# Kernel tuning notes

Measured on AMD Instinct MI355X. Metric: run time of the kernel, lower is better.

## Reference

```python
import jax, jax.numpy as jnp
import numpy as np

B, N, C, H = 8, 4096, 512, 8
DH = C // H
EPS = 1e-12  # torch F.normalize eps


def setup_inputs() -> dict:
    key = jax.random.key(0)
    ks = jax.random.split(key, 5)
    x = jax.random.normal(ks[0], (B, N, C), dtype=jnp.float32)
    y = jax.random.normal(ks[1], (B, N, 256), dtype=jnp.float32)
    kv_w = jax.random.normal(ks[2], (2 * C, C), dtype=jnp.float32) / np.sqrt(C)
    q_w = jax.random.normal(ks[3], (C, 256), dtype=jnp.float32) / np.sqrt(256)
    proj_w = jax.random.normal(ks[4], (C, C), dtype=jnp.float32) / np.sqrt(C)
    proj_b = jnp.zeros((C,), dtype=jnp.float32)
    temperature = jnp.ones((H, 1, 1), dtype=jnp.float32)
    return {"x": x, "y": y, "kv_w": kv_w, "q_w": q_w,
            "proj_w": proj_w, "proj_b": proj_b, "temperature": temperature}


def _l2norm(t):
    # torch F.normalize(dim=-1): t / max(||t||, eps)
    n = jnp.sqrt(jnp.sum(t * t, axis=-1, keepdims=True))
    return t / jnp.maximum(n, EPS)


def reference(x, y, kv_w, q_w, proj_w, proj_b, temperature):
    b, n, c = x.shape
    dh = c // H
    kv = (x @ kv_w.T).reshape(b, n, 2, H, dh)
    k = kv[:, :, 0].transpose(0, 2, 3, 1)  # [B,H,dh,N]
    v = kv[:, :, 1].transpose(0, 2, 3, 1)  # [B,H,dh,N]
    q = (y @ q_w.T).reshape(b, n, H, dh).transpose(0, 2, 3, 1)  # [B,H,dh,N]
    q = _l2norm(q)
    k = _l2norm(k)
    attn = jnp.einsum('bhdn,bhen->bhde', q, k) * temperature  # [B,H,dh,dh]
    attn = jax.nn.softmax(attn, axis=-1)
    out = jnp.einsum('bhde,bhen->bhdn', attn, v)  # [B,H,dh,N]
    out = out.transpose(0, 3, 1, 2).reshape(b, n, c)  # [B,N,C]
    return out @ proj_w.T + proj_b
```

## Files before the change

### kernel.cpp

```cpp
#include <hip/hip_runtime.h>
#include <stdint.h>

typedef unsigned short u16;
typedef unsigned int u32;
typedef __attribute__((ext_vector_type(8))) short bf16x8;
typedef __attribute__((ext_vector_type(4))) float f32x4;

typedef __attribute__((address_space(1))) const u32* gas_p;
typedef __attribute__((address_space(3))) u32* las_p;

__device__ __forceinline__ float bf2f(u16 u) {
    union { u32 u; float f; } v; v.u = ((u32)u) << 16; return v.f;
}
__device__ __forceinline__ u16 f2bf(float f) {
    union { __bf16 b; u16 u; } v; v.b = (__bf16)f; return v.u;
}
__device__ __forceinline__ uint4 cvt8(float4 a, float4 b) {
    union { u16 h[8]; uint4 v; } o;
    o.h[0] = f2bf(a.x); o.h[1] = f2bf(a.y); o.h[2] = f2bf(a.z); o.h[3] = f2bf(a.w);
    o.h[4] = f2bf(b.x); o.h[5] = f2bf(b.y); o.h[6] = f2bf(b.z); o.h[7] = f2bf(b.w);
    return o.v;
}
__device__ __forceinline__ void gl_lds16(const u16* g, u16* l) {
    __builtin_amdgcn_global_load_lds((gas_p)g, (las_p)l, 16, 0, 0);
}
__device__ __forceinline__ bool is_f32(const void* tp) {
    return *(const u32*)tp == 0x3F800000u;
}

__launch_bounds__(256)
__global__ void convert_inputs(const void* __restrict__ kvwi, const void* __restrict__ qwi,
                               const void* __restrict__ pwi, const void* __restrict__ pbi,
                               const void* __restrict__ tpi,
                               u16* __restrict__ kvwb, u16* __restrict__ qwb,
                               u16* __restrict__ pwb, u16* __restrict__ pbb,
                               float* __restrict__ tempf)
{
    const bool f32m = is_f32(tpi);
    long c = (long)blockIdx.x * 256 + threadIdx.x;
    const void* src; u16* dst; long local;
    if      (c < 65536)  { src = kvwi; dst = kvwb; local = c; }
    else if (c < 81920)  { src = qwi;  dst = qwb;  local = c - 65536; }
    else if (c < 114688) { src = pwi;  dst = pwb;  local = c - 81920; }
    else if (c < 114752) { src = pbi;  dst = pbb;  local = c - 114688; }
    else if (c == 114752) {
        for (int i = 0; i < 8; i++)
            tempf[i] = f32m ? ((const float*)tpi)[i] : bf2f(((const u16*)tpi)[i]);
        return;
    } else return;

    long e0 = local * 8;
    if (f32m) {
        const float* s = (const float*)src + e0;
        *(uint4*)(dst + e0) = cvt8(*(const float4*)s, *(const float4*)(s + 4));
    } else {
        *(uint4*)(dst + e0) = *(const uint4*)((const u16*)src + e0);
    }
}

__launch_bounds__(256)
__global__ void gemm_qkT(const void* __restrict__ xv, const void* __restrict__ yv,
                         const u16* __restrict__ kvwb, const u16* __restrict__ qwb,
                         u16* __restrict__ qT, u16* __restrict__ kT,
                         const void* __restrict__ tp)
{
    __shared__ __align__(16) u16 smem[17408];
    u16 (*As)[128][32] = (u16(*)[128][32])smem;
    u16 (*Bs)[128][32] = (u16(*)[128][32])(smem + 8192);

    const int id = blockIdx.x;
    const int xcd = id & 7, j = id >> 3;
    const int z = j >> 7, jj = j & 127;
    const int n0 = (jj & 3) * 128;
    const int m0 = (xcd * 32 + (jj >> 2)) * 128;

    const void* Av = z ? xv : yv;
    const u16* Bw  = z ? kvwb : qwb;
    u16* T         = z ? kT : qT;
    const int K    = z ? 512 : 256;

    const bool f32m = is_f32(tp);
    const int t  = threadIdx.x;
    const int w = t >> 6, lane = t & 63, quad = lane >> 4, l16 = lane & 15;
    const int wm = (w >> 1) * 64, wn = (w & 1) * 64;

    f32x4 acc[4][4];
#pragma unroll
    for (int i = 0; i < 4; i++)
#pragma unroll
        for (int jx = 0; jx < 4; jx++) acc[i][jx] = (f32x4){0.f, 0.f, 0.f, 0.f};

    const int slot = t & 3, srow = t >> 2;
    const int csw = (slot ^ ((t >> 3) & 3)) * 8;
    const int dst = slot * 8;
    const int qsw = (quad ^ ((l16 >> 1) & 3)) * 8;

    const float* Af = (const float*)Av;
    const u16*   Ab = (const u16*)Av;
    const long a0r = (long)(m0 + srow) * K + csw;
    const long a1r = (long)(m0 + srow + 64) * K + csw;
    const long b0r = (long)(n0 + srow) * K + csw;
    const long b1r = (long)(n0 + srow + 64) * K + csw;

    if (f32m) {
        float4 p0 = *(const float4*)&Af[a0r], p1 = *(const float4*)&Af[a0r + 4];
        float4 p2 = *(const float4*)&Af[a1r], p3 = *(const float4*)&Af[a1r + 4];
        *(uint4*)&As[0][srow][dst]      = cvt8(p0, p1);
        *(uint4*)&As[0][srow + 64][dst] = cvt8(p2, p3);
    } else {
        gl_lds16(&Ab[a0r], &As[0][srow][dst]);
        gl_lds16(&Ab[a1r], &As[0][srow + 64][dst]);
    }
    gl_lds16(&Bw[b0r], &Bs[0][srow][dst]);
    gl_lds16(&Bw[b1r], &Bs[0][srow + 64][dst]);
    __syncthreads();

    const int nk = K >> 5;
    for (int kk = 0; kk < nk; kk++) {
        const int cur = kk & 1, nxt = cur ^ 1;
        const int k1 = (kk + 1) << 5;
        const bool more = (kk + 1 < nk);
        float4 la0, la1, lb0, lb1;
        if (more) {
            if (f32m) {
                la0 = *(const float4*)&Af[a0r + k1];
                la1 = *(const float4*)&Af[a0r + k1 + 4];
                lb0 = *(const float4*)&Af[a1r + k1];
                lb1 = *(const float4*)&Af[a1r + k1 + 4];
            } else {
                gl_lds16(&Ab[a0r + k1], &As[nxt][srow][dst]);
                gl_lds16(&Ab[a1r + k1], &As[nxt][srow + 64][dst]);
            }
            gl_lds16(&Bw[b0r + k1], &Bs[nxt][srow][dst]);
            gl_lds16(&Bw[b1r + k1], &Bs[nxt][srow + 64][dst]);
        }
        bf16x8 af[4], bfv[4];
#pragma unroll
        for (int i = 0; i < 4; i++) af[i]  = *(const bf16x8*)&As[cur][wm + i * 16 + l16][qsw];
#pragma unroll
        for (int jx = 0; jx < 4; jx++) bfv[jx] = *(const bf16x8*)&Bs[cur][wn + jx * 16 + l16][qsw];
#pragma unroll
        for (int i = 0; i < 4; i++)
#pragma unroll
            for (int jx = 0; jx < 4; jx++)
                acc[i][jx] = __builtin_amdgcn_mfma_f32_16x16x32_bf16(af[i], bfv[jx], acc[i][jx], 0, 0, 0);
        if (more && f32m) {
            *(uint4*)&As[nxt][srow][dst]      = cvt8(la0, la1);
            *(uint4*)&As[nxt][srow + 64][dst] = cvt8(lb0, lb1);
        }
        __syncthreads();
    }

    u16 (*Cs)[136] = (u16(*)[136])smem;
#pragma unroll
    for (int i = 0; i < 4; i++)
#pragma unroll
        for (int jx = 0; jx < 4; jx++)
#pragma unroll
            for (int r = 0; r < 4; r++)
                Cs[wn + jx * 16 + l16][wm + i * 16 + quad * 4 + r] = f2bf(acc[i][jx][r]);
    __syncthreads();
    const int nrow = t >> 1, mh = (t & 1) * 64;
    const int gn = n0 + nrow;
    const int gm = m0 + mh;
    const int bb = gm >> 12, tok = gm & 4095;
    const long tbase = ((long)(bb * 512 + gn)) * 4096 + tok;
#pragma unroll
    for (int v8 = 0; v8 < 8; v8++)
        *(uint4*)&T[tbase + v8 * 8] = *(uint4*)&Cs[nrow][mh + v8 * 8];
}

__launch_bounds__(256)
__global__ void gram_kernel(const u16* __restrict__ qT, const u16* __restrict__ kT,
                            float* __restrict__ pQK, float* __restrict__ pDQ,
                            float* __restrict__ pDK)
{
    const int nc = blockIdx.x, bh = blockIdx.y;
    const int t = threadIdx.x, w = t >> 6, lane = t & 63;
    const int quad = lane >> 4, l16 = lane & 15;

    __shared__ float red[4][64][64];
    __shared__ float dql[4][64];
    __shared__ float dkl[4][64];

    const u16* qb = qT + (long)bh * 64 * 4096;
    const u16* kb = kT + (long)bh * 64 * 4096;

    f32x4 g[4][4], gq[4], gk[4];
#pragma unroll
    for (int i = 0; i < 4; i++) {
        gq[i] = (f32x4){0.f, 0.f, 0.f, 0.f};
        gk[i] = (f32x4){0.f, 0.f, 0.f, 0.f};
#pragma unroll
        for (int j = 0; j < 4; j++) g[i][j] = (f32x4){0.f, 0.f, 0.f, 0.f};
    }

#pragma unroll
    for (int ks = 0; ks < 4; ks++) {
        const int n = nc * 512 + w * 128 + ks * 32 + quad * 8;
        bf16x8 aq[4], bk[4];
#pragma unroll
        for (int i = 0; i < 4; i++) aq[i] = *(const bf16x8*)&qb[(long)(i * 16 + l16) * 4096 + n];
#pragma unroll
        for (int j = 0; j < 4; j++) bk[j] = *(const bf16x8*)&kb[(long)(j * 16 + l16) * 4096 + n];
#pragma unroll
        for (int i = 0; i < 4; i++)
#pragma unroll
            for (int j = 0; j < 4; j++)
                g[i][j] = __builtin_amdgcn_mfma_f32_16x16x32_bf16(aq[i], bk[j], g[i][j], 0, 0, 0);
#pragma unroll
        for (int i = 0; i < 4; i++) {
            gq[i] = __builtin_amdgcn_mfma_f32_16x16x32_bf16(aq[i], aq[i], gq[i], 0, 0, 0);
            gk[i] = __builtin_amdgcn_mfma_f32_16x16x32_bf16(bk[i], bk[i], gk[i], 0, 0, 0);
        }
    }

#pragma unroll
    for (int i = 0; i < 4; i++)
#pragma unroll
        for (int j = 0; j < 4; j++)
#pragma unroll
            for (int r = 0; r < 4; r++)
                red[w][i * 16 + quad * 4 + r][j * 16 + l16] = g[i][j][r];
    if ((l16 >> 2) == quad) {
        const int rr = l16 & 3;
#pragma unroll
        for (int i = 0; i < 4; i++) {
            float dq = 0.f, dk = 0.f;
#pragma unroll
            for (int r = 0; r < 4; r++)
                if (r == rr) { dq = gq[i][r]; dk = gk[i][r]; }
            dql[w][i * 16 + l16] = dq;
            dkl[w][i * 16 + l16] = dk;
        }
    }
    __syncthreads();

    const long obase = (long)(nc * 64 + bh);
    const int e = t & 63, d0 = (t >> 6) * 16;
    float* o = pQK + obase * 4096;
#pragma unroll
    for (int dd = 0; dd < 16; dd++) {
        int d = d0 + dd;
        o[d * 64 + e] = red[0][d][e] + red[1][d][e] + red[2][d][e] + red[3][d][e];
    }
    if (t < 64) {
        pDQ[obase * 64 + t] = dql[0][t] + dql[1][t] + dql[2][t] + dql[3][t];
        pDK[obase * 64 + t] = dkl[0][t] + dkl[1][t] + dkl[2][t] + dkl[3][t];
    }
}

__launch_bounds__(256)
__global__ void attn_kernel(const float* __restrict__ pQK, const float* __restrict__ pDQ,
                            const float* __restrict__ pDK, const float* __restrict__ tempf,
                            u16* __restrict__ attnT)
{
    const int bh = blockIdx.x;
    const int t = threadIdx.x, w = t >> 6, l = t & 63;
    __shared__ float G[64][65];
    __shared__ float rq[64], rk[64];

#pragma unroll
    for (int ii = 0; ii < 16; ii++) {
        int i = w * 16 + ii;
        float s = 0.f;
#pragma unroll
        for (int nc = 0; nc < 8; nc++) s += pQK[((long)(nc * 64 + bh)) * 4096 + i * 64 + l];
        G[i][l] = s;
    }
    if (t < 64) {
        float sq = 0.f, sk = 0.f;
#pragma unroll
        for (int nc = 0; nc < 8; nc++) {
            sq += pDQ[(nc * 64 + bh) * 64 + t];
            sk += pDK[(nc * 64 + bh) * 64 + t];
        }
        rq[t] = 1.f / fmaxf(sqrtf(sq), 1e-12f);
        rk[t] = 1.f / fmaxf(sqrtf(sk), 1e-12f);
    }
    __syncthreads();

    if (t < 64) {
        const float invq = tempf[bh & 7] * rq[t];
        float mx = -1e30f;
        float row[64];
#pragma unroll
        for (int e = 0; e < 64; e++) {
            float s = G[t][e] * invq * rk[e];
            row[e] = s;
            mx = fmaxf(mx, s);
        }
        float sum = 0.f;
#pragma unroll
        for (int e = 0; e < 64; e++) {
            float p = __expf(row[e] - mx);
            row[e] = p;
            sum += p;
        }
        float inv = 1.f / sum;
#pragma unroll
        for (int e = 0; e < 64; e++)
            attnT[((long)bh * 64 + e) * 64 + t] = f2bf(row[e] * inv);
    }
}

__launch_bounds__(256)
__global__ void wcomb_kernel(const u16* __restrict__ attnT, const u16* __restrict__ pwb,
                             u16* __restrict__ Wc)
{
    const int cc = blockIdx.x, bh = blockIdx.y;
    const int b = bh >> 3, h = bh & 7;
    const int t = threadIdx.x, w = t >> 6, lane = t & 63;
    const int quad = lane >> 4, l16 = lane & 15;
    const int cb = cc * 128 + w * 32;

    f32x4 acc[2][4];
#pragma unroll
    for (int i = 0; i < 2; i++)
#pragma unroll
        for (int j = 0; j < 4; j++) acc[i][j] = (f32x4){0.f, 0.f, 0.f, 0.f};

#pragma unroll
    for (int ks = 0; ks < 2; ks++) {
        const int k = ks * 32 + quad * 8;
        bf16x8 af[2], bfr[4];
#pragma unroll
        for (int i = 0; i < 2; i++)
            af[i] = *(const bf16x8*)&pwb[(long)(cb + i * 16 + l16) * 512 + h * 64 + k];
#pragma unroll
        for (int j = 0; j < 4; j++)
            bfr[j] = *(const bf16x8*)&attnT[((long)bh * 64 + j * 16 + l16) * 64 + k];
#pragma unroll
        for (int i = 0; i < 2; i++)
#pragma unroll
            for (int j = 0; j < 4; j++)
                acc[i][j] = __builtin_amdgcn_mfma_f32_16x16x32_bf16(af[i], bfr[j], acc[i][j], 0, 0, 0);
    }

#pragma unroll
    for (int i = 0; i < 2; i++)
#pragma unroll
        for (int j = 0; j < 4; j++)
#pragma unroll
            for (int r = 0; r < 4; r++) {
                int c = cb + i * 16 + quad * 4 + r;
                int e = j * 16 + l16;
                Wc[((long)(b * 512 + c)) * 512 + h * 64 + e] = f2bf(acc[i][j][r]);
            }
}

__launch_bounds__(256)
__global__ void transpose_kv(const u16* __restrict__ in, u16* __restrict__ out)
{
    __shared__ __align__(16) u16 ts[64][72];
    const int bx = blockIdx.x * 64;
    const int by = blockIdx.y * 64;
    const int t = threadIdx.x;
    const int r = t >> 3, c0 = (t & 7) * 8;
#pragma unroll
    for (int p = 0; p < 2; p++)
        *(uint4*)&ts[r + p * 32][c0] = *(const uint4*)&in[(long)(by + r + p * 32) * 512 + bx + c0];
    __syncthreads();
#pragma unroll
    for (int p = 0; p < 2; p++) {
        int rr = r + p * 32;
        union { u16 h[8]; uint4 v; } tmp;
#pragma unroll
        for (int c = 0; c < 8; c++) tmp.h[c] = ts[c0 + c][rr];
        *(uint4*)&out[(long)(bx + rr) * 512 + by + c0] = tmp.v;
    }
}

__launch_bounds__(256)
__global__ void gemm_bt(const u16* __restrict__ A, const u16* __restrict__ B,
                        u16* __restrict__ C,
                        int K, long sA, long sB, long sC)
{
    __shared__ __align__(16) u16 smem[17408];
    u16 (*As)[128][32] = (u16(*)[128][32])smem;
    u16 (*Bs)[128][32] = (u16(*)[128][32])(smem + 8192);

    const int id = blockIdx.x;
    const int z = id & 7, jj = id >> 3;
    const int n0 = (jj & 3) * 128;
    const int m0 = (jj >> 2) * 128;
    const int t  = threadIdx.x;
    A += (long)z * sA;
    B += (long)z * sB;
    C += (long)z * sC;

    const int w = t >> 6, lane = t & 63, quad = lane >> 4, l16 = lane & 15;
    const int wm = (w >> 1) * 64, wn = (w & 1) * 64;

    f32x4 acc[4][4];
#pragma unroll
    for (int i = 0; i < 4; i++)
#pragma unroll
        for (int j = 0; j < 4; j++) acc[i][j] = (f32x4){0.f, 0.f, 0.f, 0.f};

    const int slot = t & 3, srow = t >> 2;
    const int csw = (slot ^ ((t >> 3) & 3)) * 8;
    const int dst = slot * 8;
    const int qsw = (quad ^ ((l16 >> 1) & 3)) * 8;

    const long a0r = (long)(m0 + srow) * K + csw;
    const long a1r = (long)(m0 + srow + 64) * K + csw;
    const long b0r = (long)(n0 + srow) * K + csw;
    const long b1r = (long)(n0 + srow + 64) * K + csw;

    gl_lds16(&A[a0r], &As[0][srow][dst]);
    gl_lds16(&A[a1r], &As[0][srow + 64][dst]);
    gl_lds16(&B[b0r], &Bs[0][srow][dst]);
    gl_lds16(&B[b1r], &Bs[0][srow + 64][dst]);
    __syncthreads();

    const int nk = K >> 5;
    for (int kk = 0; kk < nk; kk++) {
        const int cur = kk & 1, nxt = cur ^ 1;
        const int k1 = (kk + 1) << 5;
        if (kk + 1 < nk) {
            gl_lds16(&A[a0r + k1], &As[nxt][srow][dst]);
            gl_lds16(&A[a1r + k1], &As[nxt][srow + 64][dst]);
            gl_lds16(&B[b0r + k1], &Bs[nxt][srow][dst]);
            gl_lds16(&B[b1r + k1], &Bs[nxt][srow + 64][dst]);
        }
        bf16x8 af[4], bfr[4];
#pragma unroll
        for (int i = 0; i < 4; i++) af[i]  = *(const bf16x8*)&As[cur][wm + i * 16 + l16][qsw];
#pragma unroll
        for (int j = 0; j < 4; j++) bfr[j] = *(const bf16x8*)&Bs[cur][wn + j * 16 + l16][qsw];
#pragma unroll
        for (int i = 0; i < 4; i++)
#pragma unroll
            for (int j = 0; j < 4; j++)
                acc[i][j] = __builtin_amdgcn_mfma_f32_16x16x32_bf16(af[i], bfr[j], acc[i][j], 0, 0, 0);
        __syncthreads();
    }

    u16 (*Cs)[136] = (u16(*)[136])smem;
#pragma unroll
    for (int i = 0; i < 4; i++)
#pragma unroll
        for (int j = 0; j < 4; j++) {
            int nn = wn + j * 16 + l16;
#pragma unroll
            for (int r = 0; r < 4; r++)
                Cs[wm + i * 16 + quad * 4 + r][nn] = f2bf(acc[i][j][r]);
        }
    __syncthreads();
    const int row = t >> 1, c0 = (t & 1) * 64;
#pragma unroll
    for (int v8 = 0; v8 < 8; v8++)
        *(uint4*)&C[(long)(m0 + row) * 512 + n0 + c0 + v8 * 8] = *(uint4*)&Cs[row][c0 + v8 * 8];
}

__launch_bounds__(256)
__global__ void gemm_out(const void* __restrict__ Av, const u16* __restrict__ B,
                         void* __restrict__ Cv, const u16* __restrict__ bias,
                         const void* __restrict__ tp)
{
    __shared__ __align__(16) u16 smem[17408];
    u16 (*As)[128][32] = (u16(*)[128][32])smem;
    u16 (*Bs)[128][32] = (u16(*)[128][32])(smem + 8192);

    const bool f32m = is_f32(tp);
    const int id = blockIdx.x;
    const int z = id & 7, jj = id >> 3;
    const int n0 = (jj & 3) * 128;
    const int m0 = (jj >> 2) * 128;
    const int t  = threadIdx.x;
    const long aoff = (long)z * 4096 * 512;
    B += (long)z * 512 * 512;

    const int w = t >> 6, lane = t & 63, quad = lane >> 4, l16 = lane & 15;
    const int wm = (w >> 1) * 64, wn = (w & 1) * 64;

    f32x4 acc[4][4];
#pragma unroll
    for (int i = 0; i < 4; i++)
#pragma unroll
        for (int j = 0; j < 4; j++) acc[i][j] = (f32x4){0.f, 0.f, 0.f, 0.f};

    const int slot = t & 3, srow = t >> 2;
    const int csw = (slot ^ ((t >> 3) & 3)) * 8;
    const int dst = slot * 8;
    const int qsw = (quad ^ ((l16 >> 1) & 3)) * 8;

    const float* Af = (const float*)Av + aoff;
    const u16*   Ab = (const u16*)Av + aoff;
    const long a0r = (long)(m0 + srow) * 512 + csw;
    const long a1r = (long)(m0 + srow + 64) * 512 + csw;
    const long b0r = (long)(n0 + srow) * 512 + csw;
    const long b1r = (long)(n0 + srow + 64) * 512 + csw;

    if (f32m) {
        float4 p0 = *(const float4*)&Af[a0r], p1 = *(const float4*)&Af[a0r + 4];
        float4 p2 = *(const float4*)&Af[a1r], p3 = *(const float4*)&Af[a1r + 4];
        *(uint4*)&As[0][srow][dst]      = cvt8(p0, p1);
        *(uint4*)&As[0][srow + 64][dst] = cvt8(p2, p3);
    } else {
        gl_lds16(&Ab[a0r], &As[0][srow][dst]);
        gl_lds16(&Ab[a1r], &As[0][srow + 64][dst]);
    }
    gl_lds16(&B[b0r], &Bs[0][srow][dst]);
    gl_lds16(&B[b1r], &Bs[0][srow + 64][dst]);
    __syncthreads();

    for (int kk = 0; kk < 16; kk++) {
        const int cur = kk & 1, nxt = cur ^ 1;
        const int k1 = (kk + 1) << 5;
        const bool more = (kk + 1 < 16);
        float4 la0, la1, lb0, lb1;
        if (more) {
            if (f32m) {
                la0 = *(const float4*)&Af[a0r + k1];
                la1 = *(const float4*)&Af[a0r + k1 + 4];
                lb0 = *(const float4*)&Af[a1r + k1];
                lb1 = *(const float4*)&Af[a1r + k1 + 4];
            } else {
                gl_lds16(&Ab[a0r + k1], &As[nxt][srow][dst]);
                gl_lds16(&Ab[a1r + k1], &As[nxt][srow + 64][dst]);
            }
            gl_lds16(&B[b0r + k1], &Bs[nxt][srow][dst]);
            gl_lds16(&B[b1r + k1], &Bs[nxt][srow + 64][dst]);
        }
        bf16x8 af[4], bfr[4];
#pragma unroll
        for (int i = 0; i < 4; i++) af[i]  = *(const bf16x8*)&As[cur][wm + i * 16 + l16][qsw];
#pragma unroll
        for (int j = 0; j < 4; j++) bfr[j] = *(const bf16x8*)&Bs[cur][wn + j * 16 + l16][qsw];
#pragma unroll
        for (int i = 0; i < 4; i++)
#pragma unroll
            for (int j = 0; j < 4; j++)
                acc[i][j] = __builtin_amdgcn_mfma_f32_16x16x32_bf16(af[i], bfr[j], acc[i][j], 0, 0, 0);
        if (more && f32m) {
            *(uint4*)&As[nxt][srow][dst]      = cvt8(la0, la1);
            *(uint4*)&As[nxt][srow + 64][dst] = cvt8(lb0, lb1);
        }
        __syncthreads();
    }

    if (f32m) {
        float (*Cf)[132] = (float(*)[132])smem;
        float* C = (float*)Cv + (long)z * 4096 * 512;
#pragma unroll
        for (int p = 0; p < 2; p++) {
            __syncthreads();
            if ((w >> 1) == p) {
#pragma unroll
                for (int i = 0; i < 4; i++)
#pragma unroll
                    for (int j = 0; j < 4; j++) {
                        int nn = wn + j * 16 + l16;
                        float bv = bf2f(bias[n0 + nn]);
#pragma unroll
                        for (int r = 0; r < 4; r++)
                            Cf[i * 16 + quad * 4 + r][nn] = acc[i][j][r] + bv;
                    }
            }
            __syncthreads();
            int row = t >> 2, cb = (t & 3) * 32;
#pragma unroll
            for (int v4 = 0; v4 < 8; v4++)
                *(float4*)&C[(long)(m0 + p * 64 + row) * 512 + n0 + cb + v4 * 4] =
                    *(float4*)&Cf[row][cb + v4 * 4];
        }
    } else {
        u16 (*Cs)[136] = (u16(*)[136])smem;
        u16* C = (u16*)Cv + (long)z * 4096 * 512;
#pragma unroll
        for (int i = 0; i < 4; i++)
#pragma unroll
            for (int j = 0; j < 4; j++) {
                int nn = wn + j * 16 + l16;
                float bv = bf2f(bias[n0 + nn]);
#pragma unroll
                for (int r = 0; r < 4; r++)
                    Cs[wm + i * 16 + quad * 4 + r][nn] = f2bf(acc[i][j][r] + bv);
            }
        __syncthreads();
        const int row = t >> 1, c0 = (t & 1) * 64;
#pragma unroll
        for (int v8 = 0; v8 < 8; v8++)
            *(uint4*)&C[(long)(m0 + row) * 512 + n0 + c0 + v8 * 8] = *(uint4*)&Cs[row][c0 + v8 * 8];
    }
}

extern "C" void kernel_launch(void* const* d_in, const int* in_sizes, int n_in,
                              void* d_out, int out_size, void* d_ws, size_t ws_size,
                              hipStream_t stream)
{
    const void* x      = d_in[0];
    const void* y      = d_in[1];
    const void* kv_w   = d_in[2];
    const void* q_w    = d_in[3];
    const void* proj_w = d_in[4];
    const void* proj_b = d_in[5];
    const void* temp   = d_in[6];

    char* ws = (char*)d_ws;
    u16*   kvwb  = (u16*)(ws);
    u16*   qwb   = (u16*)(ws + 1048576);
    u16*   pwb   = (u16*)(ws + 1310720);
    u16*   pbb   = (u16*)(ws + 1835008);
    float* tempf = (float*)(ws + 1836032);
    u16*   qT    = (u16*)(ws + 2097152);
    u16*   kT    = (u16*)(ws + 35651584);
    float* pQK   = (float*)(ws + 69206016);
    float* pDQ   = (float*)(ws + 77594624);
    float* pDK   = (float*)(ws + 77725696);
    u16*   attnT = (u16*)(ws + 77856768);
    u16*   Wc    = (u16*)(ws + 78381056);
    u16*   kvvT  = (u16*)(ws + 82575360);
    u16*   Wfin  = (u16*)(ws + 83099648);

    convert_inputs<<<449, 256, 0, stream>>>(kv_w, q_w, proj_w, proj_b, temp,
                                            kvwb, qwb, pwb, pbb, tempf);
    gemm_qkT<<<2048, 256, 0, stream>>>(x, y, kvwb, qwb, qT, kT, temp);
    gram_kernel<<<dim3(8, 64), 256, 0, stream>>>(qT, kT, pQK, pDQ, pDK);
    attn_kernel<<<64, 256, 0, stream>>>(pQK, pDQ, pDK, tempf, attnT);
    wcomb_kernel<<<dim3(4, 64), 256, 0, stream>>>(attnT, pwb, Wc);
    transpose_kv<<<dim3(8, 8), 256, 0, stream>>>(kvwb + 512 * 512, kvvT);
    gemm_bt<<<128, 256, 0, stream>>>(Wc, kvvT, Wfin,
                                     512, (long)512 * 512, 0, (long)512 * 512);
    gemm_out<<<1024, 256, 0, stream>>>(x, Wfin, d_out, pbb, temp);
}
```

Measured before the change: 301.7 us.

## Deepen GEMM K-loop prefetch to two stages with triple-buffered LDS

```diff
diff --git a/kernel.cpp b/kernel.cpp
--- a/kernel.cpp
+++ b/kernel.cpp
@@ -27,6 +27,9 @@
 __device__ __forceinline__ bool is_f32(const void* tp) {
     return *(const u32*)tp == 0x3F800000u;
 }
+
+#define S_VM(N) asm volatile("s_waitcnt vmcnt(" #N ")" ::: "memory")
+#define S_LG0() asm volatile("s_waitcnt lgkmcnt(0)" ::: "memory")
 
 __launch_bounds__(256)
 __global__ void convert_inputs(const void* __restrict__ kvwi, const void* __restrict__ qwi,
@@ -64,7 +67,7 @@
                          u16* __restrict__ qT, u16* __restrict__ kT,
                          const void* __restrict__ tp)
 {
-    __shared__ __align__(16) u16 smem[17408];
+    __shared__ __align__(16) u16 smem[20480];
     u16 (*As)[128][32] = (u16(*)[128][32])smem;
     u16 (*Bs)[128][32] = (u16(*)[128][32])(smem + 8192);
 
@@ -78,9 +81,10 @@
     const u16* Bw  = z ? kvwb : qwb;
     u16* T         = z ? kT : qT;
     const int K    = z ? 512 : 256;
+    const int nk   = K >> 5;
 
     const bool f32m = is_f32(tp);
-    const int t  = threadIdx.x;
+    const int t = threadIdx.x;
     const int w = t >> 6, lane = t & 63, quad = lane >> 4, l16 = lane & 15;
     const int wm = (w >> 1) * 64, wn = (w & 1) * 64;
 
@@ -102,55 +106,105 @@
     const long b0r = (long)(n0 + srow) * K + csw;
     const long b1r = (long)(n0 + srow + 64) * K + csw;
 
+#define QK_READ_MFMA(KK)                                                        \
+    {                                                                           \
+        bf16x8 af_[4], bf_[4];                                                  \
+        _Pragma("unroll")                                                       \
+        for (int i = 0; i < 4; i++)                                             \
+            af_[i] = *(const bf16x8*)&As[(KK) & 1][wm + i * 16 + l16][qsw];     \
+        _Pragma("unroll")                                                       \
+        for (int jx = 0; jx < 4; jx++)                                          \
+            bf_[jx] = *(const bf16x8*)&Bs[(KK) % 3][wn + jx * 16 + l16][qsw];   \
+        _Pragma("unroll")                                                       \
+        for (int i = 0; i < 4; i++)                                             \
+            _Pragma("unroll")                                                   \
+            for (int jx = 0; jx < 4; jx++)                                      \
+                acc[i][jx] = __builtin_amdgcn_mfma_f32_16x16x32_bf16(           \
+                    af_[i], bf_[jx], acc[i][jx], 0, 0, 0);                      \
+    }
+
     if (f32m) {
-        float4 p0 = *(const float4*)&Af[a0r], p1 = *(const float4*)&Af[a0r + 4];
-        float4 p2 = *(const float4*)&Af[a1r], p3 = *(const float4*)&Af[a1r + 4];
-        *(uint4*)&As[0][srow][dst]      = cvt8(p0, p1);
-        *(uint4*)&As[0][srow + 64][dst] = cvt8(p2, p3);
+        float4 ra0[4], ra1[4];
+        ra0[0] = *(const float4*)&Af[a0r];      ra0[1] = *(const float4*)&Af[a0r + 4];
+        ra0[2] = *(const float4*)&Af[a1r];      ra0[3] = *(const float4*)&Af[a1r + 4];
+        gl_lds16(&Bw[b0r], &Bs[0][srow][dst]);
+        gl_lds16(&Bw[b1r], &Bs[0][srow + 64][dst]);
+        ra1[0] = *(const float4*)&Af[a0r + 32]; ra1[1] = *(const float4*)&Af[a0r + 36];
+        ra1[2] = *(const float4*)&Af[a1r + 32]; ra1[3] = *(const float4*)&Af[a1r + 36];
+        gl_lds16(&Bw[b0r + 32], &Bs[1][srow][dst]);
+        gl_lds16(&Bw[b1r + 32], &Bs[1][srow + 64][dst]);
+        *(uint4*)&As[0][srow][dst]      = cvt8(ra0[0], ra0[1]);
+        *(uint4*)&As[0][srow + 64][dst] = cvt8(ra0[2], ra0[3]);
+        S_VM(6); S_LG0();
+        __builtin_amdgcn_s_barrier();
+
+#define QK_BODY_F32(KK, RISS, RCVT)                                             \
+    {                                                                           \
+        if ((KK) + 2 < nk) {                                                    \
+            const long o_ = (long)((KK) + 2) * 32;                              \
+            RISS[0] = *(const float4*)&Af[a0r + o_];                            \
+            RISS[1] = *(const float4*)&Af[a0r + o_ + 4];                        \
+            RISS[2] = *(const float4*)&Af[a1r + o_];                            \
+            RISS[3] = *(const float4*)&Af[a1r + o_ + 4];                        \
+            gl_lds16(&Bw[b0r + o_], &Bs[((KK) + 2) % 3][srow][dst]);            \
+            gl_lds16(&Bw[b1r + o_], &Bs[((KK) + 2) % 3][srow + 64][dst]);       \
+        }                                                                       \
+        QK_READ_MFMA(KK);                                                       \
+        if ((KK) + 1 < nk) {                                                    \
+            *(uint4*)&As[((KK) + 1) & 1][srow][dst]      = cvt8(RCVT[0], RCVT[1]); \
+            *(uint4*)&As[((KK) + 1) & 1][srow + 64][dst] = cvt8(RCVT[2], RCVT[3]); \
+            S_LG0();                                                            \
+            S_VM(6);                                                            \
+            __builtin_amdgcn_s_barrier();                                       \
+        }                                                                       \
+    }
+        for (int kk = 0; kk < nk; kk += 2) {
+            QK_BODY_F32(kk, ra0, ra1);
+            QK_BODY_F32(kk + 1, ra1, ra0);
+        }
+#undef QK_BODY_F32
     } else {
-        gl_lds16(&Ab[a0r], &As[0][srow][dst]);
-        gl_lds16(&Ab[a1r], &As[0][srow + 64][dst]);
-    }
-    gl_lds16(&Bw[b0r], &Bs[0][srow][dst]);
-    gl_lds16(&Bw[b1r], &Bs[0][srow + 64][dst]);
+        uint4 ua0[2], ua1[2];
+        ua0[0] = *(const uint4*)&Ab[a0r];
+        ua0[1] = *(const uint4*)&Ab[a1r];
+        gl_lds16(&Bw[b0r], &Bs[0][srow][dst]);
+        gl_lds16(&Bw[b1r], &Bs[0][srow + 64][dst]);
+        ua1[0] = *(const uint4*)&Ab[a0r + 32];
+        ua1[1] = *(const uint4*)&Ab[a1r + 32];
+        gl_lds16(&Bw[b0r + 32], &Bs[1][srow][dst]);
+        gl_lds16(&Bw[b1r + 32], &Bs[1][srow + 64][dst]);
+        *(uint4*)&As[0][srow][dst]      = ua0[0];
+        *(uint4*)&As[0][srow + 64][dst] = ua0[1];
+        S_VM(4); S_LG0();
+        __builtin_amdgcn_s_barrier();
+
+#define QK_BODY_B16(KK, RISS, RCVT)                                             \
+    {                                                                           \
+        if ((KK) + 2 < nk) {                                                    \
+            const long o_ = (long)((KK) + 2) * 32;                              \
+            RISS[0] = *(const uint4*)&Ab[a0r + o_];                             \
+            RISS[1] = *(const uint4*)&Ab[a1r + o_];                             \
+            gl_lds16(&Bw[b0r + o_], &Bs[((KK) + 2) % 3][srow][dst]);            \
+            gl_lds16(&Bw[b1r + o_], &Bs[((KK) + 2) % 3][srow + 64][dst]);       \
+        }                                                                       \
+        QK_READ_MFMA(KK);                                                       \
+        if ((KK) + 1 < nk) {                                                    \
+            *(uint4*)&As[((KK) + 1) & 1][srow][dst]      = RCVT[0];             \
+            *(uint4*)&As[((KK) + 1) & 1][srow + 64][dst] = RCVT[1];             \
+            S_LG0();                                                            \
+            S_VM(4);                                                            \
+            __builtin_amdgcn_s_barrier();                                       \
+        }                                                                       \
+    }
+        for (int kk = 0; kk < nk; kk += 2) {
+            QK_BODY_B16(kk, ua0, ua1);
+            QK_BODY_B16(kk + 1, ua1, ua0);
+        }
+#undef QK_BODY_B16
+    }
+#undef QK_READ_MFMA
+
     __syncthreads();
-
-    const int nk = K >> 5;
-    for (int kk = 0; kk < nk; kk++) {
-        const int cur = kk & 1, nxt = cur ^ 1;
-        const int k1 = (kk + 1) << 5;
-        const bool more = (kk + 1 < nk);
-        float4 la0, la1, lb0, lb1;
-        if (more) {
-            if (f32m) {
-                la0 = *(const float4*)&Af[a0r + k1];
-                la1 = *(const float4*)&Af[a0r + k1 + 4];
-                lb0 = *(const float4*)&Af[a1r + k1];
-                lb1 = *(const float4*)&Af[a1r + k1 + 4];
-            } else {
-                gl_lds16(&Ab[a0r + k1], &As[nxt][srow][dst]);
-                gl_lds16(&Ab[a1r + k1], &As[nxt][srow + 64][dst]);
-            }
-            gl_lds16(&Bw[b0r + k1], &Bs[nxt][srow][dst]);
-            gl_lds16(&Bw[b1r + k1], &Bs[nxt][srow + 64][dst]);
-        }
-        bf16x8 af[4], bfv[4];
-#pragma unroll
-        for (int i = 0; i < 4; i++) af[i]  = *(const bf16x8*)&As[cur][wm + i * 16 + l16][qsw];
-#pragma unroll
-        for (int jx = 0; jx < 4; jx++) bfv[jx] = *(const bf16x8*)&Bs[cur][wn + jx * 16 + l16][qsw];
-#pragma unroll
-        for (int i = 0; i < 4; i++)
-#pragma unroll
-            for (int jx = 0; jx < 4; jx++)
-                acc[i][jx] = __builtin_amdgcn_mfma_f32_16x16x32_bf16(af[i], bfv[jx], acc[i][jx], 0, 0, 0);
-        if (more && f32m) {
-            *(uint4*)&As[nxt][srow][dst]      = cvt8(la0, la1);
-            *(uint4*)&As[nxt][srow + 64][dst] = cvt8(lb0, lb1);
-        }
-        __syncthreads();
-    }
-
     u16 (*Cs)[136] = (u16(*)[136])smem;
 #pragma unroll
     for (int i = 0; i < 4; i++)
@@ -376,9 +430,9 @@
                         u16* __restrict__ C,
                         int K, long sA, long sB, long sC)
 {
-    __shared__ __align__(16) u16 smem[17408];
-    u16 (*As)[128][32] = (u16(*)[128][32])smem;
-    u16 (*Bs)[128][32] = (u16(*)[128][32])(smem + 8192);
+    __shared__ __align__(16) u16 smem[24576];
+    u16 (*As3)[128][32] = (u16(*)[128][32])smem;
+    u16 (*Bs3)[128][32] = (u16(*)[128][32])(smem + 12288);
 
     const int id = blockIdx.x;
     const int z = id & 7, jj = id >> 3;
@@ -408,35 +462,45 @@
     const long b0r = (long)(n0 + srow) * K + csw;
     const long b1r = (long)(n0 + srow + 64) * K + csw;
 
-    gl_lds16(&A[a0r], &As[0][srow][dst]);
-    gl_lds16(&A[a1r], &As[0][srow + 64][dst]);
-    gl_lds16(&B[b0r], &Bs[0][srow][dst]);
-    gl_lds16(&B[b1r], &Bs[0][srow + 64][dst]);
-    __syncthreads();
-
     const int nk = K >> 5;
+    gl_lds16(&A[a0r], &As3[0][srow][dst]);
+    gl_lds16(&A[a1r], &As3[0][srow + 64][dst]);
+    gl_lds16(&B[b0r], &Bs3[0][srow][dst]);
+    gl_lds16(&B[b1r], &Bs3[0][srow + 64][dst]);
+    gl_lds16(&A[a0r + 32], &As3[1][srow][dst]);
+    gl_lds16(&A[a1r + 32], &As3[1][srow + 64][dst]);
+    gl_lds16(&B[b0r + 32], &Bs3[1][srow][dst]);
+    gl_lds16(&B[b1r + 32], &Bs3[1][srow + 64][dst]);
+    S_VM(4);
+    __builtin_amdgcn_s_barrier();
+
     for (int kk = 0; kk < nk; kk++) {
-        const int cur = kk & 1, nxt = cur ^ 1;
-        const int k1 = (kk + 1) << 5;
-        if (kk + 1 < nk) {
-            gl_lds16(&A[a0r + k1], &As[nxt][srow][dst]);
-            gl_lds16(&A[a1r + k1], &As[nxt][srow + 64][dst]);
-            gl_lds16(&B[b0r + k1], &Bs[nxt][srow][dst]);
-            gl_lds16(&B[b1r + k1], &Bs[nxt][srow + 64][dst]);
-        }
+        if (kk + 2 < nk) {
+            const long o = (long)(kk + 2) * 32;
+            const int bi = (kk + 2) % 3;
+            gl_lds16(&A[a0r + o], &As3[bi][srow][dst]);
+            gl_lds16(&A[a1r + o], &As3[bi][srow + 64][dst]);
+            gl_lds16(&B[b0r + o], &Bs3[bi][srow][dst]);
+            gl_lds16(&B[b1r + o], &Bs3[bi][srow + 64][dst]);
+        }
+        const int cb3 = kk % 3;
         bf16x8 af[4], bfr[4];
 #pragma unroll
-        for (int i = 0; i < 4; i++) af[i]  = *(const bf16x8*)&As[cur][wm + i * 16 + l16][qsw];
-#pragma unroll
-        for (int j = 0; j < 4; j++) bfr[j] = *(const bf16x8*)&Bs[cur][wn + j * 16 + l16][qsw];
+        for (int i = 0; i < 4; i++) af[i]  = *(const bf16x8*)&As3[cb3][wm + i * 16 + l16][qsw];
+#pragma unroll
+        for (int j = 0; j < 4; j++) bfr[j] = *(const bf16x8*)&Bs3[cb3][wn + j * 16 + l16][qsw];
 #pragma unroll
         for (int i = 0; i < 4; i++)
 #pragma unroll
             for (int j = 0; j < 4; j++)
                 acc[i][j] = __builtin_amdgcn_mfma_f32_16x16x32_bf16(af[i], bfr[j], acc[i][j], 0, 0, 0);
-        __syncthreads();
-    }
-
+        if (kk + 1 < nk) {
+            S_VM(4);
+            __builtin_amdgcn_s_barrier();
+        }
+    }
+
+    __syncthreads();
     u16 (*Cs)[136] = (u16(*)[136])smem;
 #pragma unroll
     for (int i = 0; i < 4; i++)
@@ -459,7 +523,7 @@
                          void* __restrict__ Cv, const u16* __restrict__ bias,
                          const void* __restrict__ tp)
 {
-    __shared__ __align__(16) u16 smem[17408];
+    __shared__ __align__(16) u16 smem[20480];
     u16 (*As)[128][32] = (u16(*)[128][32])smem;
     u16 (*Bs)[128][32] = (u16(*)[128][32])(smem + 8192);
 
@@ -492,54 +556,105 @@
     const long a1r = (long)(m0 + srow + 64) * 512 + csw;
     const long b0r = (long)(n0 + srow) * 512 + csw;
     const long b1r = (long)(n0 + srow + 64) * 512 + csw;
+    const int nk = 16;
+
+#define GO_READ_MFMA(KK)                                                        \
+    {                                                                           \
+        bf16x8 af_[4], bf_[4];                                                  \
+        _Pragma("unroll")                                                       \
+        for (int i = 0; i < 4; i++)                                             \
+            af_[i] = *(const bf16x8*)&As[(KK) & 1][wm + i * 16 + l16][qsw];     \
+        _Pragma("unroll")                                                       \
+        for (int jx = 0; jx < 4; jx++)                                          \
+            bf_[jx] = *(const bf16x8*)&Bs[(KK) % 3][wn + jx * 16 + l16][qsw];   \
+        _Pragma("unroll")                                                       \
+        for (int i = 0; i < 4; i++)                                             \
+            _Pragma("unroll")                                                   \
+            for (int jx = 0; jx < 4; jx++)                                      \
+                acc[i][jx] = __builtin_amdgcn_mfma_f32_16x16x32_bf16(           \
+                    af_[i], bf_[jx], acc[i][jx], 0, 0, 0);                      \
+    }
 
     if (f32m) {
-        float4 p0 = *(const float4*)&Af[a0r], p1 = *(const float4*)&Af[a0r + 4];
-        float4 p2 = *(const float4*)&Af[a1r], p3 = *(const float4*)&Af[a1r + 4];
-        *(uint4*)&As[0][srow][dst]      = cvt8(p0, p1);
-        *(uint4*)&As[0][srow + 64][dst] = cvt8(p2, p3);
+        float4 ra0[4], ra1[4];
+        ra0[0] = *(const float4*)&Af[a0r];      ra0[1] = *(const float4*)&Af[a0r + 4];
+        ra0[2] = *(const float4*)&Af[a1r];      ra0[3] = *(const float4*)&Af[a1r + 4];
+        gl_lds16(&B[b0r], &Bs[0][srow][dst]);
+        gl_lds16(&B[b1r], &Bs[0][srow + 64][dst]);
+        ra1[0] = *(const float4*)&Af[a0r + 32]; ra1[1] = *(const float4*)&Af[a0r + 36];
+        ra1[2] = *(const float4*)&Af[a1r + 32]; ra1[3] = *(const float4*)&Af[a1r + 36];
+        gl_lds16(&B[b0r + 32], &Bs[1][srow][dst]);
+        gl_lds16(&B[b1r + 32], &Bs[1][srow + 64][dst]);
+        *(uint4*)&As[0][srow][dst]      = cvt8(ra0[0], ra0[1]);
+        *(uint4*)&As[0][srow + 64][dst] = cvt8(ra0[2], ra0[3]);
+        S_VM(6); S_LG0();
+        __builtin_amdgcn_s_barrier();
+
+#define GO_BODY_F32(KK, RISS, RCVT)                                             \
+    {                                                                           \
+        if ((KK) + 2 < nk) {                                                    \
+            const long o_ = (long)((KK) + 2) * 32;                              \
+            RISS[0] = *(const float4*)&Af[a0r + o_];                            \
+            RISS[1] = *(const float4*)&Af[a0r + o_ + 4];                        \
+            RISS[2] = *(const float4*)&Af[a1r + o_];                            \
+            RISS[3] = *(const float4*)&Af[a1r + o_ + 4];                        \
+            gl_lds16(&B[b0r + o_], &Bs[((KK) + 2) % 3][srow][dst]);             \
+            gl_lds16(&B[b1r + o_], &Bs[((KK) + 2) % 3][srow + 64][dst]);        \
+        }                                                                       \
+        GO_READ_MFMA(KK);                                                       \
+        if ((KK) + 1 < nk) {                                                    \
+            *(uint4*)&As[((KK) + 1) & 1][srow][dst]      = cvt8(RCVT[0], RCVT[1]); \
+            *(uint4*)&As[((KK) + 1) & 1][srow + 64][dst] = cvt8(RCVT[2], RCVT[3]); \
+            S_LG0();                                                            \
+            S_VM(6);                                                            \
+            __builtin_amdgcn_s_barrier();                                       \
+        }                                                                       \
+    }
+        for (int kk = 0; kk < nk; kk += 2) {
+            GO_BODY_F32(kk, ra0, ra1);
+            GO_BODY_F32(kk + 1, ra1, ra0);
+        }
+#undef GO_BODY_F32
     } else {
-        gl_lds16(&Ab[a0r], &As[0][srow][dst]);
-        gl_lds16(&Ab[a1r], &As[0][srow + 64][dst]);
-    }
-    gl_lds16(&B[b0r], &Bs[0][srow][dst]);
-    gl_lds16(&B[b1r], &Bs[0][srow + 64][dst]);
-    __syncthreads();
-
-    for (int kk = 0; kk < 16; kk++) {
-        const int cur = kk & 1, nxt = cur ^ 1;
-        const int k1 = (kk + 1) << 5;
-        const bool more = (kk + 1 < 16);
-        float4 la0, la1, lb0, lb1;
-        if (more) {
-            if (f32m) {
-                la0 = *(const float4*)&Af[a0r + k1];
-                la1 = *(const float4*)&Af[a0r + k1 + 4];
-                lb0 = *(const float4*)&Af[a1r + k1];
-                lb1 = *(const float4*)&Af[a1r + k1 + 4];
-            } else {
-                gl_lds16(&Ab[a0r + k1], &As[nxt][srow][dst]);
-                gl_lds16(&Ab[a1r + k1], &As[nxt][srow + 64][dst]);
-            }
-            gl_lds16(&B[b0r + k1], &Bs[nxt][srow][dst]);
-            gl_lds16(&B[b1r + k1], &Bs[nxt][srow + 64][dst]);
-        }
-        bf16x8 af[4], bfr[4];
-#pragma unroll
-        for (int i = 0; i < 4; i++) af[i]  = *(const bf16x8*)&As[cur][wm + i * 16 + l16][qsw];
-#pragma unroll
-        for (int j = 0; j < 4; j++) bfr[j] = *(const bf16x8*)&Bs[cur][wn + j * 16 + l16][qsw];
-#pragma unroll
-        for (int i = 0; i < 4; i++)
-#pragma unroll
-            for (int j = 0; j < 4; j++)
-                acc[i][j] = __builtin_amdgcn_mfma_f32_16x16x32_bf16(af[i], bfr[j], acc[i][j], 0, 0, 0);
-        if (more && f32m) {
-            *(uint4*)&As[nxt][srow][dst]      = cvt8(la0, la1);
-            *(uint4*)&As[nxt][srow + 64][dst] = cvt8(lb0, lb1);
-        }
-        __syncthreads();
-    }
+        uint4 ua0[2], ua1[2];
+        ua0[0] = *(const uint4*)&Ab[a0r];
+        ua0[1] = *(const uint4*)&Ab[a1r];
+        gl_lds16(&B[b0r], &Bs[0][srow][dst]);
+        gl_lds16(&B[b1r], &Bs[0][srow + 64][dst]);
+        ua1[0] = *(const uint4*)&Ab[a0r + 32];
+        ua1[1] = *(const uint4*)&Ab[a1r + 32];
+        gl_lds16(&B[b0r + 32], &Bs[1][srow][dst]);
+        gl_lds16(&B[b1r + 32], &Bs[1][srow + 64][dst]);
+        *(uint4*)&As[0][srow][dst]      = ua0[0];
+        *(uint4*)&As[0][srow + 64][dst] = ua0[1];
+        S_VM(4); S_LG0();
+        __builtin_amdgcn_s_barrier();
+
+#define GO_BODY_B16(KK, RISS, RCVT)                                             \
+    {                                                                           \
+        if ((KK) + 2 < nk) {                                                    \
+            const long o_ = (long)((KK) + 2) * 32;                              \
+            RISS[0] = *(const uint4*)&Ab[a0r + o_];                             \
+            RISS[1] = *(const uint4*)&Ab[a1r + o_];                             \
+            gl_lds16(&B[b0r + o_], &Bs[((KK) + 2) % 3][srow][dst]);             \
+            gl_lds16(&B[b1r + o_], &Bs[((KK) + 2) % 3][srow + 64][dst]);        \
+        }                                                                       \
+        GO_READ_MFMA(KK);                                                       \
+        if ((KK) + 1 < nk) {                                                    \
+            *(uint4*)&As[((KK) + 1) & 1][srow][dst]      = RCVT[0];             \
+            *(uint4*)&As[((KK) + 1) & 1][srow + 64][dst] = RCVT[1];             \
+            S_LG0();                                                            \
+            S_VM(4);                                                            \
+            __builtin_amdgcn_s_barrier();                                       \
+        }                                                                       \
+    }
+        for (int kk = 0; kk < nk; kk += 2) {
+            GO_BODY_B16(kk, ua0, ua1);
+            GO_BODY_B16(kk + 1, ua1, ua0);
+        }
+#undef GO_BODY_B16
+    }
+#undef GO_READ_MFMA
 
     if (f32m) {
         float (*Cf)[132] = (float(*)[132])smem;
@@ -567,6 +682,7 @@
                     *(float4*)&Cf[row][cb + v4 * 4];
         }
     } else {
+        __syncthreads();
         u16 (*Cs)[136] = (u16(*)[136])smem;
         u16* C = (u16*)Cv + (long)z * 4096 * 512;
 #pragma unroll
```

Result: slower. 310.7 us (+3.0%).
